# Optimization experiments

Measured on AMD Instinct MI355X. Metric: run time of the kernel, lower is better.

## Reference

```python
import jax, jax.numpy as jnp
import numpy as np
import math

B, T, INP_DIM, OUT_DIM = 2, 4096, 1, 64
DEPTH, D_MODEL, N_HEADS, D_FF = 4, 512, 8, 2048
D_HEAD = D_MODEL // N_HEADS
EPS = 1e-5


def setup_inputs() -> dict:
    key = jax.random.key(0)
    ks = jax.random.split(key, 16)
    s = 0.02
    inp = {
        "x_in": jax.random.normal(ks[0], (B, T, INP_DIM), dtype=jnp.float32),
        "inp_w": jax.random.normal(ks[1], (INP_DIM, D_MODEL), dtype=jnp.float32) * s,
        "inp_b": jnp.zeros((D_MODEL,), dtype=jnp.float32),
        "pos_emb": jax.random.normal(ks[2], (T, D_MODEL), dtype=jnp.float32) * s,
        "ln1_g": jnp.ones((DEPTH, D_MODEL), dtype=jnp.float32),
        "ln1_b": jnp.zeros((DEPTH, D_MODEL), dtype=jnp.float32),
        "qkv_w": jax.random.normal(ks[3], (DEPTH, D_MODEL, 3 * D_MODEL), dtype=jnp.float32) * s,
        "proj_w": jax.random.normal(ks[4], (DEPTH, D_MODEL, D_MODEL), dtype=jnp.float32) * s,
        "ln2_g": jnp.ones((DEPTH, D_MODEL), dtype=jnp.float32),
        "ln2_b": jnp.zeros((DEPTH, D_MODEL), dtype=jnp.float32),
        "fc1_w": jax.random.normal(ks[5], (DEPTH, D_MODEL, D_FF), dtype=jnp.float32) * s,
        "fc2_w": jax.random.normal(ks[6], (DEPTH, D_FF, D_MODEL), dtype=jnp.float32) * s,
        "lnf_g": jnp.ones((D_MODEL,), dtype=jnp.float32),
        "lnf_b": jnp.zeros((D_MODEL,), dtype=jnp.float32),
        "head_w": jax.random.normal(ks[7], (D_MODEL, OUT_DIM), dtype=jnp.float32) * s,
        "head_b": jnp.zeros((OUT_DIM,), dtype=jnp.float32),
    }
    return inp


def _layernorm(x, g, b):
    mu = jnp.mean(x, axis=-1, keepdims=True)
    var = jnp.mean(jnp.square(x - mu), axis=-1, keepdims=True)
    return (x - mu) * jax.lax.rsqrt(var + EPS) * g + b


def _attn(x, qkv_w, proj_w):
    Bx, Tx, d = x.shape
    qkv = x @ qkv_w  # [B,T,3d]
    q, k, v = jnp.split(qkv, 3, axis=-1)
    q = q.reshape(Bx, Tx, N_HEADS, D_HEAD)
    k = k.reshape(Bx, Tx, N_HEADS, D_HEAD)
    v = v.reshape(Bx, Tx, N_HEADS, D_HEAD)
    scores = jnp.einsum('bqhd,bkhd->bhqk', q, k) / math.sqrt(D_HEAD)
    causal = jnp.tril(jnp.ones((Tx, Tx), dtype=bool))
    scores = jnp.where(causal, scores, -jnp.inf)
    attn = jax.nn.softmax(scores, axis=-1)
    out = jnp.einsum('bhqk,bkhd->bqhd', attn, v).reshape(Bx, Tx, d)
    return out @ proj_w


def reference(x_in, inp_w, inp_b, pos_emb, ln1_g, ln1_b, qkv_w, proj_w,
              ln2_g, ln2_b, fc1_w, fc2_w, lnf_g, lnf_b, head_w, head_b):
    x = x_in @ inp_w + inp_b + pos_emb[None, :, :]  # [B,T,d]
    for l in range(DEPTH):
        x = x + _attn(_layernorm(x, ln1_g[l], ln1_b[l]), qkv_w[l], proj_w[l])
        h = _layernorm(x, ln2_g[l], ln2_b[l])
        h = jax.nn.gelu(h @ fc1_w[l], approximate=False) @ fc2_w[l]
        x = x + h
    h = _layernorm(x, lnf_g, lnf_b)
    return h @ head_w + head_b  # [B,T,out_dim]
```

## Files before the change

kernel.cpp:

```cpp
#include <hip/hip_runtime.h>
#include <math.h>

typedef unsigned short u16;
typedef unsigned int u32;

#define B_ 2
#define T_ 4096
#define DM 512
#define NH 8
#define DH 64
#define DFF 2048
#define MTOT (B_*T_)

#define SCALEQ 0.18033688011112042f

using f32x4  = __attribute__((ext_vector_type(4))) float;
using f32x16 = __attribute__((ext_vector_type(16))) float;
using bf16x8 = __attribute__((ext_vector_type(8))) short;
typedef unsigned int u32x2 __attribute__((ext_vector_type(2)));

__device__ __forceinline__ float b2f(u16 u) {
  union { u32 u; float f; } v; v.u = ((u32)u) << 16; return v.f;
}
__device__ __forceinline__ u16 f2b(float f) {
  union { float f; u32 u; } v; v.f = f;
  u32 r = v.u + 0x7FFFu + ((v.u >> 16) & 1u);
  return (u16)(r >> 16);
}
__device__ __forceinline__ u32 cvtpk(float lo, float hi) {
  u32 r;
  asm("v_cvt_pk_bf16_f32 %0, %1, %2" : "=v"(r) : "v"(lo), "v"(hi));
  return r;
}
#if __has_builtin(__builtin_amdgcn_exp2f)
#define EXP2(x) __builtin_amdgcn_exp2f(x)
#else
#define EXP2(x) __expf((x) * 0.6931471805599453f)
#endif
#if __has_builtin(__builtin_amdgcn_rcpf)
#define RCP(x) __builtin_amdgcn_rcpf(x)
#else
#define RCP(x) (1.0f / (x))
#endif

__device__ __forceinline__ void gload_lds(const u16* g, u16* l) {
  __builtin_amdgcn_global_load_lds(
      (const __attribute__((address_space(1))) void*)g,
      (__attribute__((address_space(3))) void*)l, 16, 0, 0);
}

__device__ __forceinline__ int lsw(int row, int col) {
  int slot = ((col >> 3) + (row >> 3) + 2 * (row & 7)) & 7;
  return (row << 6) + (slot << 3) + (col & 7);
}

__device__ __forceinline__ void ln_finish(
    float* xr, float v[8], const float* g, const float* bet,
    u16* y, size_t yoff, int lane, bool writeX) {
  if (writeX) {
    float4 w0; w0.x = v[0]; w0.y = v[1]; w0.z = v[2]; w0.w = v[3];
    float4 w1; w1.x = v[4]; w1.y = v[5]; w1.z = v[6]; w1.w = v[7];
    *(float4*)xr = w0;
    *(float4*)(xr + 4) = w1;
  }
  float s = 0.f;
#pragma unroll
  for (int j = 0; j < 8; j++) s += v[j];
#pragma unroll
  for (int off = 32; off; off >>= 1) s += __shfl_xor(s, off);
  float mu = s * (1.0f / DM);
  float q = 0.f;
#pragma unroll
  for (int j = 0; j < 8; j++) { float e = v[j] - mu; q += e * e; }
#pragma unroll
  for (int off = 32; off; off >>= 1) q += __shfl_xor(q, off);
  float rs = rsqrtf(q * (1.0f / DM) + 1e-5f);
  float4 g0 = *(const float4*)(g + lane * 8);
  float4 g1 = *(const float4*)(g + lane * 8 + 4);
  float4 p0 = *(const float4*)(bet + lane * 8);
  float4 p1 = *(const float4*)(bet + lane * 8 + 4);
  float gg[8] = {g0.x, g0.y, g0.z, g0.w, g1.x, g1.y, g1.z, g1.w};
  float pp[8] = {p0.x, p0.y, p0.z, p0.w, p1.x, p1.y, p1.z, p1.w};
  uint4 st;
  st.x = cvtpk((v[0]-mu)*rs*gg[0]+pp[0], (v[1]-mu)*rs*gg[1]+pp[1]);
  st.y = cvtpk((v[2]-mu)*rs*gg[2]+pp[2], (v[3]-mu)*rs*gg[3]+pp[3]);
  st.z = cvtpk((v[4]-mu)*rs*gg[4]+pp[4], (v[5]-mu)*rs*gg[5]+pp[5]);
  st.w = cvtpk((v[6]-mu)*rs*gg[6]+pp[6], (v[7]-mu)*rs*gg[7]+pp[7]);
  *(uint4*)(y + yoff) = st;
}

__global__ __launch_bounds__(256) void embln_k(
    const float* __restrict__ x_in, const float* __restrict__ w,
    const float* __restrict__ bias, const float* __restrict__ pos,
    const float* __restrict__ g, const float* __restrict__ bet,
    float* __restrict__ x, u16* __restrict__ y) {
  int wid = threadIdx.x >> 6, lane = threadIdx.x & 63;
  int row = blockIdx.x * 4 + wid;
  int t = row & (T_ - 1);
  float xs = x_in[row];
  const float* pr = pos + (size_t)t * DM + lane * 8;
  float4 p0 = *(const float4*)pr;
  float4 p1 = *(const float4*)(pr + 4);
  float4 w0 = *(const float4*)(w + lane * 8);
  float4 w1 = *(const float4*)(w + lane * 8 + 4);
  float4 b0 = *(const float4*)(bias + lane * 8);
  float4 b1 = *(const float4*)(bias + lane * 8 + 4);
  float v[8];
  v[0] = xs * w0.x + b0.x + p0.x; v[1] = xs * w0.y + b0.y + p0.y;
  v[2] = xs * w0.z + b0.z + p0.z; v[3] = xs * w0.w + b0.w + p0.w;
  v[4] = xs * w1.x + b1.x + p1.x; v[5] = xs * w1.y + b1.y + p1.y;
  v[6] = xs * w1.z + b1.z + p1.z; v[7] = xs * w1.w + b1.w + p1.w;
  float* xr = x + (size_t)row * DM + lane * 8;
  ln_finish(xr, v, g, bet, y, (size_t)row * DM + lane * 8, lane, true);
}

template<int NP>
__global__ __launch_bounds__(256) void ln_k(
    float* __restrict__ x, const u16* __restrict__ P,
    const float* __restrict__ g, const float* __restrict__ bet,
    u16* __restrict__ y) {
  int wid = threadIdx.x >> 6, lane = threadIdx.x & 63;
  int row = blockIdx.x * 4 + wid;
  float* xr = x + (size_t)row * DM + lane * 8;
  float4 a0 = *(const float4*)xr;
  float4 a1 = *(const float4*)(xr + 4);
  float v[8] = {a0.x, a0.y, a0.z, a0.w, a1.x, a1.y, a1.z, a1.w};
  if (NP > 0) {
#pragma unroll
    for (int s = 0; s < NP; s++) {
      const u16* pr = P + (size_t)s * MTOT * DM + (size_t)row * DM + lane * 8;
      uint4 pv = *(const uint4*)pr;
      const u16* px = (const u16*)&pv;
#pragma unroll
      for (int j = 0; j < 8; j++) v[j] += b2f(px[j]);
    }
  }
  ln_finish(xr, v, g, bet, y, (size_t)row * DM + lane * 8, lane, NP > 0);
}

__global__ __launch_bounds__(256) void wconv_k(
    const float* __restrict__ W, u16* __restrict__ Wt, int K, int N) {
  __shared__ float tile[32][33];
  const float* Wl = W + (size_t)blockIdx.z * K * N;
  u16* Wtl = Wt + (size_t)blockIdx.z * K * N;
  int k0 = blockIdx.x * 32, n0 = blockIdx.y * 32;
  int r = threadIdx.x >> 3, c4 = (threadIdx.x & 7) * 4;
  *(float4*)&tile[r][c4] = *(const float4*)(Wl + (size_t)(k0 + r) * N + n0 + c4);
  __syncthreads();
  uint2 st;
  st.x = cvtpk(tile[c4 + 0][r], tile[c4 + 1][r]);
  st.y = cvtpk(tile[c4 + 2][r], tile[c4 + 3][r]);
  *(uint2*)(Wtl + (size_t)(n0 + r) * K + k0 + c4) = st;
}

template<int EPI>
__global__ __launch_bounds__(256) void gemm_k(
    const u16* __restrict__ A, const u16* __restrict__ Bt,
    u16* __restrict__ Cb, float* __restrict__ Cf,
    int M, int N, int K, int Kslice, int scale_cols) {
  __shared__ u16 As[2][128][32];
  __shared__ u16 Bs[2][128][32];
  int tid = threadIdx.x;
  int lane = tid & 63, wid = tid >> 6;
  int wr = wid >> 1, wc = wid & 1;
  int nwg = gridDim.x * gridDim.y;
  int flat = blockIdx.y * gridDim.x + blockIdx.x;
  int swz = (flat & 7) * (nwg >> 3) + (flat >> 3);
  int bx = swz % gridDim.x, by = swz / gridDim.x;
  int m0 = by * 128, n0 = bx * 128;
  int kbeg = blockIdx.z * Kslice;
  if (EPI == 4) Cb += (size_t)blockIdx.z * M * N;
  f32x4 acc[4][4] = {};
  int rsub = lane >> 2, ksub = (lane & 3) * 8;
  const u16* Ab = A  + (size_t)(m0 + wid * 32 + rsub) * K + kbeg + ksub;
  const u16* Bb = Bt + (size_t)(n0 + wid * 32 + rsub) * K + kbeg + ksub;
#define GSTAGE(BUF, KO) { \
    gload_lds(Ab + (KO), &As[BUF][wid * 32][0]); \
    gload_lds(Ab + (size_t)16 * K + (KO), &As[BUF][wid * 32 + 16][0]); \
    gload_lds(Bb + (KO), &Bs[BUF][wid * 32][0]); \
    gload_lds(Bb + (size_t)16 * K + (KO), &Bs[BUF][wid * 32 + 16][0]); }
  GSTAGE(0, 0);
  __syncthreads();
  int r = lane & 15, kc = (lane >> 4) * 8;
  for (int k0 = 0; k0 < Kslice; k0 += 32) {
    int cur = (k0 >> 5) & 1;
    if (k0 + 32 < Kslice) GSTAGE(cur ^ 1, k0 + 32);
    bf16x8 af[4], bfr[4];
#pragma unroll
    for (int m = 0; m < 4; m++) af[m]  = *(const bf16x8*)&As[cur][wr*64 + m*16 + r][kc];
#pragma unroll
    for (int n = 0; n < 4; n++) bfr[n] = *(const bf16x8*)&Bs[cur][wc*64 + n*16 + r][kc];
#pragma unroll
    for (int m = 0; m < 4; m++)
#pragma unroll
      for (int n = 0; n < 4; n++)
        acc[m][n] = __builtin_amdgcn_mfma_f32_16x16x32_bf16(af[m], bfr[n], acc[m][n], 0, 0, 0);
    __syncthreads();
  }
  int r4 = (lane >> 4) * 4, cN = lane & 15;
#pragma unroll
  for (int m = 0; m < 4; m++) {
#pragma unroll
    for (int n = 0; n < 4; n++) {
      int col = n0 + wc*64 + n*16 + cN;
#pragma unroll
      for (int i = 0; i < 4; i++) {
        int row = m0 + wr*64 + m*16 + r4 + i;
        size_t off = (size_t)row * N + col;
        float v = acc[m][n][i];
        if (EPI == 0) {
          if (col < scale_cols) v *= SCALEQ;
          Cb[off] = f2b(v);
        } else if (EPI == 1) {
          Cf[off] += v;
        } else if (EPI == 4) {
          Cb[off] = f2b(v);
        } else {
          float e = EXP2(v * (2.3022082f + 0.10294324f * v * v));
          Cb[off] = f2b(v * (1.0f - RCP(e + 1.0f)));
        }
      }
    }
  }
}

#if __has_builtin(__builtin_amdgcn_permlane32_swap)
#define PLSWAP(A, B, O0, O1) { \
    u32x2 r_ = __builtin_amdgcn_permlane32_swap((A), (B), false, false); \
    O0 = r_.x; O1 = r_.y; }
#else
#define PLSWAP(A, B, O0, O1) { \
    u32 as_ = __shfl_xor((u32)(A), 32), bs_ = __shfl_xor((u32)(B), 32); \
    O0 = hh ? bs_ : (A); O1 = hh ? (B) : as_; }
#endif

__global__ __launch_bounds__(256) void attn_k(const u16* __restrict__ qkv,
                                              u16* __restrict__ Opart,
                                              float* __restrict__ ml) {
  __shared__ u16 Ks[2][64 * 64];
  __shared__ u16 Vt[2][64 * 64];
  int tid = threadIdx.x;
  int w = tid >> 6, l = tid & 63;
  int hh = l >> 5, c = l & 31;
  int flat = blockIdx.y * 144 + blockIdx.x;
  int swz = (flat & 7) * 288 + (flat >> 3);
  int bh = swz / 144, slot = swz - bh * 144;
  int g = 0;
  while (2 * (g + 1) * (g + 2) <= slot) g++;
  int s2 = slot - 2 * g * (g + 1);
  int qb = 4 * g + s2 / (g + 1);
  int ck = s2 - (s2 / (g + 1)) * (g + 1);
  int ntot = 2 * qb + 2;
  int kt0 = ck * 8;
  int kt1 = kt0 + 8 < ntot ? kt0 + 8 : ntot;
  int b = bh >> 3, hd = bh & 7;
  int q0w = qb * 128 + w * 32;
  int q_abs = q0w + c;
  size_t base = (size_t)b * T_ * 1536;
  bf16x8 qf[4];
  const u16* qp = qkv + base + (size_t)q_abs * 1536 + hd * 64 + hh * 8;
#pragma unroll
  for (int kk = 0; kk < 4; kk++) qf[kk] = *(const bf16x8*)(qp + kk * 16);
  f32x16 oa0 = {}, oa1 = {};
  float m_run = -1e30f, l_run = 0.f;
  int sp = tid >> 3, d8 = (tid & 7) * 8;
  int r0 = sp * 2, r1 = r0 + 1;
  const u16* kvbase = qkv + base + DM + hd * 64 + d8;
  uint4 kreg0, kreg1, vreg0, vreg1;
#define AGLOAD(KT) { \
    const u16* s0_ = kvbase + (size_t)((KT) * 64 + r0) * 1536; \
    kreg0 = *(const uint4*)s0_; vreg0 = *(const uint4*)(s0_ + DM); \
    const u16* s1_ = s0_ + 1536; \
    kreg1 = *(const uint4*)s1_; vreg1 = *(const uint4*)(s1_ + DM); }
  AGLOAD(kt0);
  for (int kt = kt0; kt < kt1; kt++) {
    u16* Kb = Ks[kt & 1];
    u16* Vb = Vt[kt & 1];
    *(uint4*)&Kb[lsw(r0, d8)] = kreg0;
    *(uint4*)&Kb[lsw(r1, d8)] = kreg1;
    {
      const u16* v0 = (const u16*)&vreg0;
      const u16* v1 = (const u16*)&vreg1;
#pragma unroll
      for (int j = 0; j < 8; j++) {
        u32 pw = (u32)v0[j] | ((u32)v1[j] << 16);
        *(u32*)&Vb[lsw(d8 + j, r0)] = pw;
      }
    }
    __syncthreads();
    if (kt + 1 < kt1) AGLOAD(kt + 1);
    if (kt * 64 > q0w + 31) continue;
    bool needMask = (kt * 64 + 63 > q0w);
    f32x16 sa0 = {}, sa1 = {};
    __builtin_amdgcn_s_setprio(1);
#pragma unroll
    for (int kk = 0; kk < 4; kk++) {
      bf16x8 ka  = *(const bf16x8*)&Kb[lsw(c,      kk * 16 + hh * 8)];
      bf16x8 kb2 = *(const bf16x8*)&Kb[lsw(32 + c, kk * 16 + hh * 8)];
      sa0 = __builtin_amdgcn_mfma_f32_32x32x16_bf16(ka,  qf[kk], sa0, 0, 0, 0);
      sa1 = __builtin_amdgcn_mfma_f32_32x32x16_bf16(kb2, qf[kk], sa1, 0, 0, 0);
    }
    __builtin_amdgcn_s_setprio(0);
    if (needMask) {
#pragma unroll
      for (int gi = 0; gi < 4; gi++)
#pragma unroll
        for (int i = 0; i < 4; i++) {
          int krow = kt * 64 + gi * 8 + hh * 4 + i;
          if (krow > q_abs)      sa0[gi * 4 + i] = -1e30f;
          if (krow + 32 > q_abs) sa1[gi * 4 + i] = -1e30f;
        }
    }
    float t[8];
#pragma unroll
    for (int r = 0; r < 8; r++)
      t[r] = fmaxf(fmaxf(sa0[r], sa0[r + 8]), fmaxf(sa1[r], sa1[r + 8]));
    float pm = fmaxf(fmaxf(fmaxf(t[0], t[1]), fmaxf(t[2], t[3])),
                     fmaxf(fmaxf(t[4], t[5]), fmaxf(t[6], t[7])));
    pm = fmaxf(pm, __shfl_xor(pm, 32));
    if (!__all(pm - m_run <= 8.0f)) {
      float mnew = fmaxf(m_run, pm);
      float corr = EXP2(m_run - mnew);
      l_run *= corr;
#pragma unroll
      for (int r = 0; r < 16; r++) { oa0[r] *= corr; oa1[r] *= corr; }
      m_run = mnew;
    }
    float sarr[16];
#pragma unroll
    for (int r = 0; r < 16; r++) {
      float e0 = EXP2(sa0[r] - m_run); sa0[r] = e0;
      float e1 = EXP2(sa1[r] - m_run); sa1[r] = e1;
      sarr[r] = e0 + e1;
    }
#pragma unroll
    for (int r = 0; r < 8; r++) sarr[r] += sarr[r + 8];
#pragma unroll
    for (int r = 0; r < 4; r++) sarr[r] += sarr[r + 4];
    float lsum = (sarr[0] + sarr[1]) + (sarr[2] + sarr[3]);
    lsum += __shfl_xor(lsum, 32);
    l_run += lsum;
    u32 Aw[8], Bw_[8];
#pragma unroll
    for (int r2 = 0; r2 < 4; r2++) {
      Aw[r2]      = cvtpk(sa0[4 * r2 + 0], sa0[4 * r2 + 1]);
      Bw_[r2]     = cvtpk(sa0[4 * r2 + 2], sa0[4 * r2 + 3]);
      Aw[4 + r2]  = cvtpk(sa1[4 * r2 + 0], sa1[4 * r2 + 1]);
      Bw_[4 + r2] = cvtpk(sa1[4 * r2 + 2], sa1[4 * r2 + 3]);
    }
    __builtin_amdgcn_s_setprio(1);
#pragma unroll
    for (int ks = 0; ks < 4; ks++) {
      int mo = (ks >> 1) * 4;
      int r2e = mo + 2 * (ks & 1), r2o = r2e + 1;
      union { u32 wd[4]; bf16x8 v; } u;
      PLSWAP(Aw[r2e], Aw[r2o], u.wd[0], u.wd[2]);
      PLSWAP(Bw_[r2e], Bw_[r2o], u.wd[1], u.wd[3]);
      bf16x8 va = *(const bf16x8*)&Vb[lsw(c,      ks * 16 + hh * 8)];
      bf16x8 vb = *(const bf16x8*)&Vb[lsw(32 + c, ks * 16 + hh * 8)];
      oa0 = __builtin_amdgcn_mfma_f32_32x32x16_bf16(va, u.v, oa0, 0, 0, 0);
      oa1 = __builtin_amdgcn_mfma_f32_32x32x16_bf16(vb, u.v, oa1, 0, 0, 0);
    }
    __builtin_amdgcn_s_setprio(0);
  }
  int sidx = bh * 144 + slot;
  u16* op = Opart + ((size_t)sidx * 128 + w * 32 + c) * 64;
#pragma unroll
  for (int gi = 0; gi < 4; gi++) {
    uint2 s0, s1;
    s0.x = cvtpk(oa0[4*gi+0], oa0[4*gi+1]);
    s0.y = cvtpk(oa0[4*gi+2], oa0[4*gi+3]);
    s1.x = cvtpk(oa1[4*gi+0], oa1[4*gi+1]);
    s1.y = cvtpk(oa1[4*gi+2], oa1[4*gi+3]);
    int d0 = gi * 8 + hh * 4;
    *(uint2*)(op + d0)      = s0;
    *(uint2*)(op + 32 + d0) = s1;
  }
  if (hh == 0) {
    float2 p; p.x = m_run; p.y = l_run;
    *(float2*)&ml[((size_t)sidx * 128 + w * 32 + c) * 2] = p;
  }
}

__global__ __launch_bounds__(256) void comb_k(
    const u16* __restrict__ Opart, const float* __restrict__ ml,
    u16* __restrict__ attno) {
  int gi = blockIdx.x * 256 + threadIdx.x;
  int d4 = (gi & 15) * 4;
  int bhq = gi >> 4;
  int bh = bhq >> 12, q = bhq & 4095;
  int qb = q >> 7, ri = q & 127;
  int g = qb >> 2;
  int nc = g + 1;
  int bs = 2 * g * (g + 1) + (qb & 3) * (g + 1);
  int s0 = bh * 144 + bs;
  float M = -1e30f;
  for (int cc = 0; cc < nc; cc++)
    M = fmaxf(M, ml[((size_t)(s0 + cc) * 128 + ri) * 2]);
  float O0 = 0.f, O1 = 0.f, O2 = 0.f, O3 = 0.f, L = 0.f;
  for (int cc = 0; cc < nc; cc++) {
    float2 p = *(const float2*)&ml[((size_t)(s0 + cc) * 128 + ri) * 2];
    float wgt = EXP2(p.x - M);
    L += p.y * wgt;
    uint2 ov = *(const uint2*)&Opart[((size_t)(s0 + cc) * 128 + ri) * 64 + d4];
    const u16* opx = (const u16*)&ov;
    O0 += b2f(opx[0]) * wgt; O1 += b2f(opx[1]) * wgt;
    O2 += b2f(opx[2]) * wgt; O3 += b2f(opx[3]) * wgt;
  }
  float invL = 1.0f / L;
  int b = bh >> 3, hd = bh & 7;
  uint2 st;
  st.x = cvtpk(O0 * invL, O1 * invL);
  st.y = cvtpk(O2 * invL, O3 * invL);
  *(uint2*)&attno[((size_t)b * T_ + q) * DM + hd * 64 + d4] = st;
}

__global__ __launch_bounds__(256) void head_k(
    const u16* __restrict__ xb, const float* __restrict__ W,
    const float* __restrict__ bias, float* __restrict__ out) {
  int wid = threadIdx.x >> 6, lane = threadIdx.x & 63;
  int row = blockIdx.x * 4 + wid;
  const u16* xr = xb + (size_t)row * DM;
  float a0 = 0.f, a1 = 0.f, a2 = 0.f, a3 = 0.f;
  for (int d = 0; d < DM; d += 8) {
    uint4 xv = *(const uint4*)(xr + d);
    const u16* xp = (const u16*)&xv;
    const float* Wp = W + (size_t)d * 64 + lane;
    a0 += b2f(xp[0]) * Wp[0];
    a1 += b2f(xp[1]) * Wp[64];
    a2 += b2f(xp[2]) * Wp[128];
    a3 += b2f(xp[3]) * Wp[192];
    a0 += b2f(xp[4]) * Wp[256];
    a1 += b2f(xp[5]) * Wp[320];
    a2 += b2f(xp[6]) * Wp[384];
    a3 += b2f(xp[7]) * Wp[448];
  }
  out[(size_t)row * 64 + lane] = a0 + a1 + a2 + a3 + bias[lane];
}

extern "C" void kernel_launch(void* const* d_in, const int* in_sizes, int n_in,
                              void* d_out, int out_size, void* d_ws, size_t ws_size,
                              hipStream_t stream) {
  (void)in_sizes; (void)n_in; (void)out_size; (void)ws_size;
  const float* x_in  = (const float*)d_in[0];
  const float* inp_w = (const float*)d_in[1];
  const float* inp_b = (const float*)d_in[2];
  const float* pos   = (const float*)d_in[3];
  const float* ln1g  = (const float*)d_in[4];
  const float* ln1b  = (const float*)d_in[5];
  const float* qkvw  = (const float*)d_in[6];
  const float* projw = (const float*)d_in[7];
  const float* ln2g  = (const float*)d_in[8];
  const float* ln2b  = (const float*)d_in[9];
  const float* fc1w  = (const float*)d_in[10];
  const float* fc2w  = (const float*)d_in[11];
  const float* lnfg  = (const float*)d_in[12];
  const float* lnfb  = (const float*)d_in[13];
  const float* headw = (const float*)d_in[14];
  const float* headb = (const float*)d_in[15];

  char* ws = (char*)d_ws;
  size_t off = 0;
  float* x     = (float*)(ws + off); off += (size_t)MTOT * DM * 4;
  u16*  lnb    = (u16*)(ws + off);   off += (size_t)MTOT * DM * 2;
  u16*  qkvb   = (u16*)(ws + off);   off += (size_t)MTOT * 3 * DM * 2;
  u16*  attno  = (u16*)(ws + off);   off += (size_t)MTOT * DM * 2;
  u16*  ff     = qkvb;
  u16*  qkvt   = (u16*)(ws + off);   off += (size_t)4 * DM * 3 * DM * 2;
  u16*  projt  = (u16*)(ws + off);   off += (size_t)4 * DM * DM * 2;
  u16*  fc1t   = (u16*)(ws + off);   off += (size_t)4 * DM * DFF * 2;
  u16*  fc2t   = (u16*)(ws + off);   off += (size_t)4 * DFF * DM * 2;
  char* shared = ws + off;
  u16*  Opart  = (u16*)shared;
  float* mlbuf = (float*)(shared + (size_t)16 * 144 * 128 * 64 * 2);
  u16*  fcp    = (u16*)shared;

  wconv_k<<<dim3(16, 48, 4), 256, 0, stream>>>(qkvw,  qkvt, DM, 3 * DM);
  wconv_k<<<dim3(16, 16, 4), 256, 0, stream>>>(projw, projt, DM, DM);
  wconv_k<<<dim3(16, 64, 4), 256, 0, stream>>>(fc1w,  fc1t, DM, DFF);
  wconv_k<<<dim3(64, 16, 4), 256, 0, stream>>>(fc2w,  fc2t, DFF, DM);

  for (int ly = 0; ly < 4; ly++) {
    if (ly == 0)
      embln_k<<<MTOT / 4, 256, 0, stream>>>(x_in, inp_w, inp_b, pos,
                                            ln1g, ln1b, x, lnb);
    else
      ln_k<2><<<MTOT / 4, 256, 0, stream>>>(x, fcp, ln1g + ly * DM, ln1b + ly * DM, lnb);
    gemm_k<0><<<dim3(12, 64), 256, 0, stream>>>(lnb, qkvt + (size_t)ly * DM * 3 * DM,
                                                qkvb, nullptr, MTOT, 3 * DM, DM, DM, DM);
    attn_k<<<dim3(144, 16), 256, 0, stream>>>(qkvb, Opart, mlbuf);
    comb_k<<<(16 * 4096 * 16) / 256, 256, 0, stream>>>(Opart, mlbuf, attno);
    gemm_k<4><<<dim3(4, 64, 2), 256, 0, stream>>>(attno, projt + (size_t)ly * DM * DM,
                                                  fcp, nullptr, MTOT, DM, DM, DM / 2, 0);
    ln_k<2><<<MTOT / 4, 256, 0, stream>>>(x, fcp, ln2g + ly * DM, ln2b + ly * DM, lnb);
    gemm_k<2><<<dim3(16, 64), 256, 0, stream>>>(lnb, fc1t + (size_t)ly * DM * DFF,
                                                ff, nullptr, MTOT, DFF, DM, DM, 0);
    gemm_k<4><<<dim3(4, 64, 2), 256, 0, stream>>>(ff, fc2t + (size_t)ly * DFF * DM,
                                                  fcp, nullptr, MTOT, DM, DFF, DFF / 2, 0);
  }
  ln_k<2><<<MTOT / 4, 256, 0, stream>>>(x, fcp, lnfg, lnfb, lnb);
  head_k<<<MTOT / 4, 256, 0, stream>>>(lnb, headw, headb, (float*)d_out);
}
```

Measured before the change: 854.3 us.

## Add 256x256-tile 8-wave GEMM kernel for QKV and FC1 projections

```diff
diff --git a/kernel.cpp b/kernel.cpp
--- a/kernel.cpp
+++ b/kernel.cpp
@@ -151,6 +151,105 @@
   st.x = cvtpk(tile[c4 + 0][r], tile[c4 + 1][r]);
   st.y = cvtpk(tile[c4 + 2][r], tile[c4 + 3][r]);
   *(uint2*)(Wtl + (size_t)(n0 + r) * K + k0 + c4) = st;
+}
+
+template<int EPI>
+__global__ __launch_bounds__(512) void gemm8_k(
+    const u16* __restrict__ A, const u16* __restrict__ Bt,
+    u16* __restrict__ Cb, int M, int N, int K, int scale_cols) {
+  __shared__ u16 Asb[2][256][64];
+  __shared__ u16 Bsb[2][256][64];
+  int tid = threadIdx.x;
+  int lane = tid & 63, wid = tid >> 6;
+  int wr = wid >> 2, wc = wid & 3;
+  int nwg = gridDim.x * gridDim.y;
+  int flat = blockIdx.y * gridDim.x + blockIdx.x;
+  int swz = (flat & 7) * (nwg >> 3) + (flat >> 3);
+  int bx = swz % gridDim.x, by = swz / gridDim.x;
+  int m0 = by * 256, n0 = bx * 256;
+  int srow = wid * 8 + (lane >> 3);
+  int sslot = (lane & 7) ^ (lane >> 3);
+  const u16* Abase = A  + (size_t)(m0 + srow) * K + sslot * 8;
+  const u16* Bbase = Bt + (size_t)(n0 + srow) * K + sslot * 8;
+  int rA = lane & 15, hi = lane >> 4, sx = lane & 7;
+  f32x4 acc[8][4] = {};
+  int nkt = K >> 6;
+#define STGA8(BUF,HALF,J,KT) gload_lds(Abase + (size_t)((HALF)*128+(J)*64)*K + (KT)*64, \
+                                       &Asb[BUF][(HALF)*128+(J)*64+wid*8][0])
+#define STGB8(BUF,HALF,J,KT) gload_lds(Bbase + (size_t)((HALF)*128+(J)*64)*K + (KT)*64, \
+                                       &Bsb[BUF][(HALF)*128+(J)*64+wid*8][0])
+#define STGH8(BUF,HT,KT) { if ((HT) < 2) { STGA8(BUF,(HT),0,KT); STGA8(BUF,(HT),1,KT); } \
+                           else          { STGB8(BUF,(HT)-2,0,KT); STGB8(BUF,(HT)-2,1,KT); } }
+  STGH8(0,0,0); STGH8(0,1,0); STGH8(0,2,0); STGH8(0,3,0);
+  for (int kt = 0; kt < nkt; kt++) {
+    const u16 (*As)[64] = Asb[kt & 1];
+    const u16 (*Bs)[64] = Bsb[kt & 1];
+    int nbuf = (kt + 1) & 1;
+    bool more = (kt + 1 < nkt);
+    if (more) {
+      STGH8(nbuf, 0, kt + 1);
+      asm volatile("s_waitcnt vmcnt(2)" ::: "memory");
+    } else {
+      asm volatile("s_waitcnt vmcnt(0)" ::: "memory");
+    }
+    asm volatile("s_barrier" ::: "memory");
+#pragma unroll
+    for (int q = 0; q < 4; q++) {
+      if (more) {
+        if (q == 0)      { STGH8(nbuf, 1, kt + 1); }
+        else if (q == 1) { STGH8(nbuf, 2, kt + 1); }
+        else if (q == 2) { STGH8(nbuf, 3, kt + 1); }
+      }
+      const int mh = q >> 1, nh = q & 1;
+      bf16x8 af[4][2], bfr[2][2];
+#pragma unroll
+      for (int fm = 0; fm < 4; fm++)
+#pragma unroll
+        for (int ks = 0; ks < 2; ks++)
+          af[fm][ks] = *(const bf16x8*)
+              &As[wr*128 + (mh*4+fm)*16 + rA][((ks*4 + hi) ^ sx) * 8];
+#pragma unroll
+      for (int fn = 0; fn < 2; fn++)
+#pragma unroll
+        for (int ks = 0; ks < 2; ks++)
+          bfr[fn][ks] = *(const bf16x8*)
+              &Bs[wc*64 + (nh*2+fn)*16 + rA][((ks*4 + hi) ^ sx) * 8];
+      asm volatile("s_barrier" ::: "memory");
+      __builtin_amdgcn_s_setprio(1);
+#pragma unroll
+      for (int fm = 0; fm < 4; fm++)
+#pragma unroll
+        for (int fn = 0; fn < 2; fn++) {
+          acc[mh*4+fm][nh*2+fn] = __builtin_amdgcn_mfma_f32_16x16x32_bf16(
+              af[fm][0], bfr[fn][0], acc[mh*4+fm][nh*2+fn], 0, 0, 0);
+          acc[mh*4+fm][nh*2+fn] = __builtin_amdgcn_mfma_f32_16x16x32_bf16(
+              af[fm][1], bfr[fn][1], acc[mh*4+fm][nh*2+fn], 0, 0, 0);
+        }
+      __builtin_amdgcn_s_setprio(0);
+      asm volatile("s_barrier" ::: "memory");
+    }
+  }
+  int r4 = (lane >> 4) * 4, cN = lane & 15;
+#pragma unroll
+  for (int fm = 0; fm < 8; fm++) {
+#pragma unroll
+    for (int fn = 0; fn < 4; fn++) {
+      int col = n0 + wc*64 + fn*16 + cN;
+#pragma unroll
+      for (int i = 0; i < 4; i++) {
+        int row = m0 + wr*128 + fm*16 + r4 + i;
+        size_t off = (size_t)row * N + col;
+        float v = acc[fm][fn][i];
+        if (EPI == 0) {
+          if (col < scale_cols) v *= SCALEQ;
+          Cb[off] = f2b(v);
+        } else {
+          float e = EXP2(v * (2.3022082f + 0.10294324f * v * v));
+          Cb[off] = f2b(v * (1.0f - RCP(e + 1.0f)));
+        }
+      }
+    }
+  }
 }
 
 template<int EPI>
@@ -208,16 +307,12 @@
         int row = m0 + wr*64 + m*16 + r4 + i;
         size_t off = (size_t)row * N + col;
         float v = acc[m][n][i];
-        if (EPI == 0) {
-          if (col < scale_cols) v *= SCALEQ;
+        if (EPI == 4) {
           Cb[off] = f2b(v);
         } else if (EPI == 1) {
           Cf[off] += v;
-        } else if (EPI == 4) {
+        } else {
           Cb[off] = f2b(v);
-        } else {
-          float e = EXP2(v * (2.3022082f + 0.10294324f * v * v));
-          Cb[off] = f2b(v * (1.0f - RCP(e + 1.0f)));
         }
       }
     }
@@ -486,15 +581,15 @@
                                             ln1g, ln1b, x, lnb);
     else
       ln_k<2><<<MTOT / 4, 256, 0, stream>>>(x, fcp, ln1g + ly * DM, ln1b + ly * DM, lnb);
-    gemm_k<0><<<dim3(12, 64), 256, 0, stream>>>(lnb, qkvt + (size_t)ly * DM * 3 * DM,
-                                                qkvb, nullptr, MTOT, 3 * DM, DM, DM, DM);
+    gemm8_k<0><<<dim3(6, 32), 512, 0, stream>>>(lnb, qkvt + (size_t)ly * DM * 3 * DM,
+                                                qkvb, MTOT, 3 * DM, DM, DM);
     attn_k<<<dim3(144, 16), 256, 0, stream>>>(qkvb, Opart, mlbuf);
     comb_k<<<(16 * 4096 * 16) / 256, 256, 0, stream>>>(Opart, mlbuf, attno);
     gemm_k<4><<<dim3(4, 64, 2), 256, 0, stream>>>(attno, projt + (size_t)ly * DM * DM,
                                                   fcp, nullptr, MTOT, DM, DM, DM / 2, 0);
     ln_k<2><<<MTOT / 4, 256, 0, stream>>>(x, fcp, ln2g + ly * DM, ln2b + ly * DM, lnb);
-    gemm_k<2><<<dim3(16, 64), 256, 0, stream>>>(lnb, fc1t + (size_t)ly * DM * DFF,
-                                                ff, nullptr, MTOT, DFF, DM, DM, 0);
+    gemm8_k<2><<<dim3(8, 32), 512, 0, stream>>>(lnb, fc1t + (size_t)ly * DM * DFF,
+                                                ff, MTOT, DFF, DM, 0);
     gemm_k<4><<<dim3(4, 64, 2), 256, 0, stream>>>(ff, fc2t + (size_t)ly * DFF * DM,
                                                   fcp, nullptr, MTOT, DM, DFF, DFF / 2, 0);
   }
```

New measurement: 905.8 us. 6.0% more time.
